# Optimization experiments

Measured on AMD Instinct MI355X. Metric: run time of the kernel, lower is better.

The kernel has to match this reference:

```python
import jax, jax.numpy as jnp
import numpy as np

N, IN_C, OUT_C = 8192, 256, 256


def setup_inputs() -> dict:
    key = jax.random.key(0)
    ks = jax.random.split(key, 12)
    p = lambda k, shape: (jax.random.normal(k, shape, jnp.float32) * 0.05)
    return {
        "X": jax.random.normal(ks[0], (IN_C,), jnp.float32),
        "head": 100,
        "tail": 7,
        "E": jax.random.uniform(ks[1], (N, N), jnp.float32),
        "H": jax.random.normal(ks[2], (N, OUT_C), jnp.float32),
        "W_x_z": p(ks[3], (IN_C, OUT_C)),
        "W_h_z": p(ks[4], (OUT_C, OUT_C)),
        "conv_z": p(ks[5], (OUT_C, OUT_C)),
        "b_z": jnp.zeros((1, OUT_C), jnp.float32),
        "W_x_r": p(ks[6], (IN_C, OUT_C)),
        "W_h_r": p(ks[7], (OUT_C, OUT_C)),
        "conv_r": p(ks[8], (OUT_C, OUT_C)),
        "b_r": jnp.zeros((1, OUT_C), jnp.float32),
        "W_x_h": p(ks[9], (IN_C, OUT_C)),
        "W_h_h": p(ks[10], (OUT_C, OUT_C)),
        "b_h": jnp.zeros((1, OUT_C), jnp.float32),
    }


def reference(X, head, tail, E, H, W_x_z, W_h_z, conv_z, b_z,
              W_x_r, W_h_r, conv_r, b_r, W_x_h, W_h_h, b_h):
    # --- edge-weight update ---
    # Original: M = 0.5*I with M[head,tail]=0.5; Ep = E with Ep[head,tail]+=1;
    # E_new = M @ Ep.  M@Ep scales every row by 0.5 and (if head!=tail) adds
    # 0.5*Ep[tail] into row `head`.  Same math, O(N^2) instead of O(N^3).
    Ep = E.at[head, tail].add(1.0)
    E_new = 0.5 * Ep
    if head != tail:  # head/tail are Python ints (static)
        E_new = E_new.at[head].add(0.5 * Ep[tail])

    h_head = H[head]                 # [OUT_C]
    agg = E_new[head] @ H            # GCN aggregation over neighbors: [OUT_C]

    Z = jax.nn.sigmoid(X @ W_x_z + h_head @ W_h_z + agg @ conv_z + b_z[0])
    R = jax.nn.sigmoid(X @ W_x_r + h_head @ W_h_r + agg @ conv_r + b_r[0])
    H_tilde = jnp.tanh(X @ W_x_h + (h_head * R) @ W_h_h + b_h[0])

    H_new = H.at[head].set(Z * h_head + (1.0 - Z) * H_tilde)
    return E_new, H_new
```

## Files before the change

### kernel.cpp

```cpp
#include <hip/hip_runtime.h>
#include <math.h>

#define NN 8192
#define CC 256
#define LOG2N 13

typedef float f32x4 __attribute__((ext_vector_type(4)));

#define ACC_Z  0
#define ACC_R  256
#define ACC_XH 512
#define ACC_HH 768

#define NAGG    128
#define NMV     20
#define CHAIN   (NAGG + NMV)
#define NSTREAM 2048

__global__ void __launch_bounds__(256) k1(
        const float* __restrict__ X, const float* __restrict__ E,
        const float* __restrict__ H,
        const int* __restrict__ dh, const int* __restrict__ dt,
        const float* __restrict__ Wxz, const float* __restrict__ Whz,
        const float* __restrict__ Cz,  const float* __restrict__ Wxr,
        const float* __restrict__ Whr, const float* __restrict__ Cr,
        const float* __restrict__ Wxh,
        float* __restrict__ acc_ws, float* __restrict__ out) {
    const int bid = blockIdx.x;
    const int t = threadIdx.x;
    const int head = dh[0], tail = dt[0];
    const size_t nn = (size_t)NN * NN;

    if (bid >= CHAIN) {
        const size_t total4 = nn >> 2;
        const size_t step = (size_t)NSTREAM * 256;
        size_t idx = (size_t)(bid - CHAIN) * 256 + t;
        for (; idx < total4; idx += 2 * step) {
            const size_t e0 = idx << 2;
            const size_t e1 = (idx + step) << 2;
            const f32x4 a = __builtin_nontemporal_load((const f32x4*)(E + e0));
            const f32x4 b = __builtin_nontemporal_load((const f32x4*)(E + e1));
            {
                f32x4 o = a * 0.5f;
                const int i = (int)(e0 >> LOG2N);
                if (i == head) {
                    const int j = (int)(e0 & (NN - 1));
                    if (head != tail) {
                        const f32x4 w = *(const f32x4*)(E + (size_t)tail * NN + j);
                        o += w * 0.5f;
                    }
                    if (tail >= j && tail < j + 4) o[tail - j] += 0.5f;
                }
                *(f32x4*)(out + e0) = o;
            }
            {
                f32x4 o = b * 0.5f;
                const int i = (int)(e1 >> LOG2N);
                if (i == head) {
                    const int j = (int)(e1 & (NN - 1));
                    if (head != tail) {
                        const f32x4 w = *(const f32x4*)(E + (size_t)tail * NN + j);
                        o += w * 0.5f;
                    }
                    if (tail >= j && tail < j + 4) o[tail - j] += 0.5f;
                }
                *(f32x4*)(out + e1) = o;
            }
        }
        return;
    }

    if (bid < NAGG) {
        __shared__ float e_sh[64];
        __shared__ f32x4 red[4][64];
        __shared__ float agg_sh[CC];
        const int i0 = bid * 64;
        if (t < 64) {
            const int i = i0 + t;
            float e = 0.5f * E[(size_t)head * NN + i];
            if (head != tail) e += 0.5f * E[(size_t)tail * NN + i];
            if (i == tail) e += 0.5f;
            e_sh[t] = e;
        }
        __syncthreads();
        const int g = t >> 6, c = (t & 63) << 2;
        f32x4 acc = {0.f, 0.f, 0.f, 0.f};
        #pragma unroll
        for (int it = 0; it < 16; ++it) {
            const int r = it * 4 + g;
            const int row = i0 + r;
            const f32x4 hv = *(const f32x4*)(H + (size_t)row * CC + c);
            acc += hv * e_sh[r];
            if (row != head)
                *(f32x4*)(out + nn + (size_t)row * CC + c) = hv;
        }
        red[g][t & 63] = acc;
        __syncthreads();
        if (g == 0) {
            const f32x4 s = red[0][t] + red[1][t] + red[2][t] + red[3][t];
            *(f32x4*)(agg_sh + (t << 2)) = s;
        }
        __syncthreads();
        float pz = 0.f, pr = 0.f;
        #pragma unroll 8
        for (int k = 0; k < CC; ++k) {
            const float a = agg_sh[k];
            pz += a * Cz[(size_t)k * CC + t];
            pr += a * Cr[(size_t)k * CC + t];
        }
        atomicAdd(&acc_ws[ACC_Z + t], pz);
        atomicAdd(&acc_ws[ACC_R + t], pr);
        return;
    }

    {
        const int mb = bid - NAGG;
        const int m = mb >> 2, q = mb & 3;
        __shared__ float v_sh[64];
        const float* W;
        float* dst;
        switch (m) {
            case 0: W = Wxz; dst = acc_ws + ACC_Z; break;
            case 1: W = Whz; dst = acc_ws + ACC_Z; break;
            case 2: W = Wxr; dst = acc_ws + ACC_R; break;
            case 3: W = Whr; dst = acc_ws + ACC_R; break;
            default: W = Wxh; dst = acc_ws + ACC_XH; break;
        }
        if (t < 64) {
            const int k = q * 64 + t;
            v_sh[t] = (m == 1 || m == 3) ? H[(size_t)head * CC + k] : X[k];
        }
        __syncthreads();
        float acc = 0.f;
        #pragma unroll
        for (int kk = 0; kk < 64; ++kk)
            acc += v_sh[kk] * W[(size_t)(q * 64 + kk) * CC + t];
        atomicAdd(&dst[t], acc);
    }
}

__global__ void __launch_bounds__(256) k2(
        const float* __restrict__ H, const int* __restrict__ dh,
        const float* __restrict__ br, const float* __restrict__ Whh,
        float* __restrict__ acc_ws) {
    __shared__ float rs_sh[CC];
    const int t = threadIdx.x;
    const int head = dh[0];
    const float sr = br[t] + acc_ws[ACC_R + t];
    const float r = 1.f / (1.f + expf(-sr));
    rs_sh[t] = H[(size_t)head * CC + t] * r;
    __syncthreads();
    const int k0 = blockIdx.x * 8;
    float acc = 0.f;
    #pragma unroll
    for (int j = 0; j < 8; ++j)
        acc += rs_sh[k0 + j] * Whh[(size_t)(k0 + j) * CC + t];
    atomicAdd(&acc_ws[ACC_HH + t], acc);
}

__global__ void __launch_bounds__(256) k3(
        const float* __restrict__ H, const int* __restrict__ dh,
        const float* __restrict__ bz, const float* __restrict__ bh,
        const float* __restrict__ acc_ws, float* __restrict__ out) {
    const int t = threadIdx.x;
    const int head = dh[0];
    const float z = 1.f / (1.f + expf(-(bz[t] + acc_ws[ACC_Z + t])));
    const float ht = tanhf(bh[t] + acc_ws[ACC_XH + t] + acc_ws[ACC_HH + t]);
    const float h = H[(size_t)head * CC + t];
    out[(size_t)NN * NN + (size_t)head * CC + t] = z * h + (1.f - z) * ht;
}

extern "C" void kernel_launch(void* const* d_in, const int* in_sizes, int n_in,
                              void* d_out, int out_size, void* d_ws, size_t ws_size,
                              hipStream_t stream) {
    const float* X    = (const float*)d_in[0];
    const int*   dh   = (const int*)d_in[1];
    const int*   dt   = (const int*)d_in[2];
    const float* E    = (const float*)d_in[3];
    const float* H    = (const float*)d_in[4];
    const float* Wxz  = (const float*)d_in[5];
    const float* Whz  = (const float*)d_in[6];
    const float* Cz   = (const float*)d_in[7];
    const float* bz   = (const float*)d_in[8];
    const float* Wxr  = (const float*)d_in[9];
    const float* Whr  = (const float*)d_in[10];
    const float* Cr   = (const float*)d_in[11];
    const float* br   = (const float*)d_in[12];
    const float* Wxh  = (const float*)d_in[13];
    const float* Whh  = (const float*)d_in[14];
    const float* bh   = (const float*)d_in[15];
    float* out = (float*)d_out;
    float* acc_ws = (float*)d_ws;

    hipMemsetAsync(acc_ws, 0, 1024 * sizeof(float), stream);
    k1<<<CHAIN + NSTREAM, 256, 0, stream>>>(
        X, E, H, dh, dt, Wxz, Whz, Cz, Wxr, Whr, Cr, Wxh, acc_ws, out);
    k2<<<32, 256, 0, stream>>>(H, dh, br, Whh, acc_ws);
    k3<<<1, 256, 0, stream>>>(H, dh, bz, bh, acc_ws, out);
}
```

Measured before the change: 112.7 us.

## Fuse GRU tail into streaming kernel with dynamic chunk scheduling and last-block finish

Merges the three launches into one kernel. Blocks first do their GRU partial matvec work, then pull fixed-size chunks of the E copy from a global atomic counter, prefetching the next chunk index. A done-counter elects the last block to compute the Whh matvec and final H row, which removes the k2/k3 launches. The grid shrinks to 2048 blocks, so the GRU work now shares blocks with the stream, and there are per-chunk atomics and a serial 256x256 matvec at the tail.

```diff
diff --git a/kernel.cpp b/kernel.cpp
--- a/kernel.cpp
+++ b/kernel.cpp
@@ -10,12 +10,13 @@
 #define ACC_Z  0
 #define ACC_R  256
 #define ACC_XH 512
-#define ACC_HH 768
-
-#define NAGG    128
-#define NMV     20
-#define CHAIN   (NAGG + NMV)
-#define NSTREAM 2048
+
+#define NAGG   128
+#define NMV    20
+#define CHAIN  (NAGG + NMV)
+#define GRID   2048
+#define CHUNK  4096
+#define NCHUNK 4096
 
 __global__ void __launch_bounds__(256) k1(
         const float* __restrict__ X, const float* __restrict__ E,
@@ -24,26 +25,101 @@
         const float* __restrict__ Wxz, const float* __restrict__ Whz,
         const float* __restrict__ Cz,  const float* __restrict__ Wxr,
         const float* __restrict__ Whr, const float* __restrict__ Cr,
-        const float* __restrict__ Wxh,
-        float* __restrict__ acc_ws, float* __restrict__ out) {
+        const float* __restrict__ Wxh, const float* __restrict__ Whh,
+        const float* __restrict__ bz, const float* __restrict__ br,
+        const float* __restrict__ bh,
+        float* __restrict__ ws, float* __restrict__ out) {
     const int bid = blockIdx.x;
     const int t = threadIdx.x;
     const int head = dh[0], tail = dt[0];
     const size_t nn = (size_t)NN * NN;
-
-    if (bid >= CHAIN) {
-        const size_t total4 = nn >> 2;
-        const size_t step = (size_t)NSTREAM * 256;
-        size_t idx = (size_t)(bid - CHAIN) * 256 + t;
-        for (; idx < total4; idx += 2 * step) {
-            const size_t e0 = idx << 2;
-            const size_t e1 = (idx + step) << 2;
+    unsigned* ctr  = (unsigned*)ws + 1024;
+    unsigned* done = (unsigned*)ws + 1056;
+
+    if (bid < NAGG) {
+        __shared__ float e_sh[64];
+        __shared__ f32x4 red[4][64];
+        __shared__ float agg_sh[CC];
+        const int i0 = bid * 64;
+        if (t < 64) {
+            const int i = i0 + t;
+            float e = 0.5f * E[(size_t)head * NN + i];
+            if (head != tail) e += 0.5f * E[(size_t)tail * NN + i];
+            if (i == tail) e += 0.5f;
+            e_sh[t] = e;
+        }
+        __syncthreads();
+        const int g = t >> 6, c = (t & 63) << 2;
+        f32x4 acc = {0.f, 0.f, 0.f, 0.f};
+        #pragma unroll
+        for (int it = 0; it < 16; ++it) {
+            const int r = it * 4 + g;
+            const int row = i0 + r;
+            const f32x4 hv = *(const f32x4*)(H + (size_t)row * CC + c);
+            acc += hv * e_sh[r];
+            if (row != head)
+                *(f32x4*)(out + nn + (size_t)row * CC + c) = hv;
+        }
+        red[g][t & 63] = acc;
+        __syncthreads();
+        if (g == 0) {
+            const f32x4 s = red[0][t] + red[1][t] + red[2][t] + red[3][t];
+            *(f32x4*)(agg_sh + (t << 2)) = s;
+        }
+        __syncthreads();
+        float pz = 0.f, pr = 0.f;
+        #pragma unroll 8
+        for (int k = 0; k < CC; ++k) {
+            const float a = agg_sh[k];
+            pz += a * Cz[(size_t)k * CC + t];
+            pr += a * Cr[(size_t)k * CC + t];
+        }
+        atomicAdd(&ws[ACC_Z + t], pz);
+        atomicAdd(&ws[ACC_R + t], pr);
+        __syncthreads();
+    } else if (bid < CHAIN) {
+        const int mb = bid - NAGG;
+        const int m = mb >> 2, q = mb & 3;
+        __shared__ float v_sh[64];
+        const float* W;
+        int dsto;
+        switch (m) {
+            case 0: W = Wxz; dsto = ACC_Z; break;
+            case 1: W = Whz; dsto = ACC_Z; break;
+            case 2: W = Wxr; dsto = ACC_R; break;
+            case 3: W = Whr; dsto = ACC_R; break;
+            default: W = Wxh; dsto = ACC_XH; break;
+        }
+        if (t < 64) {
+            const int k = q * 64 + t;
+            v_sh[t] = (m == 1 || m == 3) ? H[(size_t)head * CC + k] : X[k];
+        }
+        __syncthreads();
+        float acc = 0.f;
+        #pragma unroll
+        for (int kk = 0; kk < 64; ++kk)
+            acc += v_sh[kk] * W[(size_t)(q * 64 + kk) * CC + t];
+        atomicAdd(&ws[dsto + t], acc);
+        __syncthreads();
+    }
+
+    __shared__ unsigned s_chunk[2];
+    if (t == 0) s_chunk[0] = atomicAdd(ctr, 1u);
+    __syncthreads();
+    unsigned cur = s_chunk[0];
+    int par = 1;
+    while (cur < NCHUNK) {
+        if (t == 0) s_chunk[par] = atomicAdd(ctr, 1u);
+        const size_t base = (size_t)cur * CHUNK + t;
+        #pragma unroll
+        for (int k = 0; k < 16; k += 2) {
+            const size_t e0 = (base + (size_t)k * 256) << 2;
+            const size_t e1 = (base + (size_t)(k + 1) * 256) << 2;
             const f32x4 a = __builtin_nontemporal_load((const f32x4*)(E + e0));
             const f32x4 b = __builtin_nontemporal_load((const f32x4*)(E + e1));
             {
                 f32x4 o = a * 0.5f;
-                const int i = (int)(e0 >> LOG2N);
-                if (i == head) {
+                if ((int)(e0 >> LOG2N) == head) {
                     const int j = (int)(e0 & (NN - 1));
                     if (head != tail) {
                         const f32x4 w = *(const f32x4*)(E + (size_t)tail * NN + j);
@@ -55,8 +131,7 @@
             }
             {
                 f32x4 o = b * 0.5f;
-                const int i = (int)(e1 >> LOG2N);
-                if (i == head) {
+                if ((int)(e1 >> LOG2N) == head) {
                     const int j = (int)(e1 & (NN - 1));
                     if (head != tail) {
                         const f32x4 w = *(const f32x4*)(E + (size_t)tail * NN + j);
@@ -67,107 +142,35 @@
                 *(f32x4*)(out + e1) = o;
             }
         }
-        return;
-    }
-
-    if (bid < NAGG) {
-        __shared__ float e_sh[64];
-        __shared__ f32x4 red[4][64];
-        __shared__ float agg_sh[CC];
-        const int i0 = bid * 64;
-        if (t < 64) {
-            const int i = i0 + t;
-            float e = 0.5f * E[(size_t)head * NN + i];
-            if (head != tail) e += 0.5f * E[(size_t)tail * NN + i];
-            if (i == tail) e += 0.5f;
-            e_sh[t] = e;
-        }
-        __syncthreads();
-        const int g = t >> 6, c = (t & 63) << 2;
-        f32x4 acc = {0.f, 0.f, 0.f, 0.f};
-        #pragma unroll
-        for (int it = 0; it < 16; ++it) {
-            const int r = it * 4 + g;
-            const int row = i0 + r;
-            const f32x4 hv = *(const f32x4*)(H + (size_t)row * CC + c);
-            acc += hv * e_sh[r];
-            if (row != head)
-                *(f32x4*)(out + nn + (size_t)row * CC + c) = hv;
-        }
-        red[g][t & 63] = acc;
-        __syncthreads();
-        if (g == 0) {
-            const f32x4 s = red[0][t] + red[1][t] + red[2][t] + red[3][t];
-            *(f32x4*)(agg_sh + (t << 2)) = s;
-        }
-        __syncthreads();
-        float pz = 0.f, pr = 0.f;
+        __syncthreads();
+        cur = s_chunk[par];
+        par ^= 1;
+    }
+
+    __shared__ int s_last;
+    if (t == 0) {
+        const unsigned old = __hip_atomic_fetch_add(done, 1u, __ATOMIC_ACQ_REL,
+                                                    __HIP_MEMORY_SCOPE_AGENT);
+        s_last = (old == GRID - 1) ? 1 : 0;
+    }
+    __syncthreads();
+    if (s_last) {
+        __shared__ float rs_sh[CC];
+        const float accR = ws[ACC_R + t];
+        const float accZ = ws[ACC_Z + t];
+        const float accXH = ws[ACC_XH + t];
+        const float h = H[(size_t)head * CC + t];
+        const float r = 1.f / (1.f + expf(-(br[t] + accR)));
+        rs_sh[t] = h * r;
+        __syncthreads();
+        float hh = 0.f;
         #pragma unroll 8
-        for (int k = 0; k < CC; ++k) {
-            const float a = agg_sh[k];
-            pz += a * Cz[(size_t)k * CC + t];
-            pr += a * Cr[(size_t)k * CC + t];
-        }
-        atomicAdd(&acc_ws[ACC_Z + t], pz);
-        atomicAdd(&acc_ws[ACC_R + t], pr);
-        return;
-    }
-
-    {
-        const int mb = bid - NAGG;
-        const int m = mb >> 2, q = mb & 3;
-        __shared__ float v_sh[64];
-        const float* W;
-        float* dst;
-        switch (m) {
-            case 0: W = Wxz; dst = acc_ws + ACC_Z; break;
-            case 1: W = Whz; dst = acc_ws + ACC_Z; break;
-            case 2: W = Wxr; dst = acc_ws + ACC_R; break;
-            case 3: W = Whr; dst = acc_ws + ACC_R; break;
-            default: W = Wxh; dst = acc_ws + ACC_XH; break;
-        }
-        if (t < 64) {
-            const int k = q * 64 + t;
-            v_sh[t] = (m == 1 || m == 3) ? H[(size_t)head * CC + k] : X[k];
-        }
-        __syncthreads();
-        float acc = 0.f;
-        #pragma unroll
-        for (int kk = 0; kk < 64; ++kk)
-            acc += v_sh[kk] * W[(size_t)(q * 64 + kk) * CC + t];
-        atomicAdd(&dst[t], acc);
-    }
-}
-
-__global__ void __launch_bounds__(256) k2(
-        const float* __restrict__ H, const int* __restrict__ dh,
-        const float* __restrict__ br, const float* __restrict__ Whh,
-        float* __restrict__ acc_ws) {
-    __shared__ float rs_sh[CC];
-    const int t = threadIdx.x;
-    const int head = dh[0];
-    const float sr = br[t] + acc_ws[ACC_R + t];
-    const float r = 1.f / (1.f + expf(-sr));
-    rs_sh[t] = H[(size_t)head * CC + t] * r;
-    __syncthreads();
-    const int k0 = blockIdx.x * 8;
-    float acc = 0.f;
-    #pragma unroll
-    for (int j = 0; j < 8; ++j)
-        acc += rs_sh[k0 + j] * Whh[(size_t)(k0 + j) * CC + t];
-    atomicAdd(&acc_ws[ACC_HH + t], acc);
-}
-
-__global__ void __launch_bounds__(256) k3(
-        const float* __restrict__ H, const int* __restrict__ dh,
-        const float* __restrict__ bz, const float* __restrict__ bh,
-        const float* __restrict__ acc_ws, float* __restrict__ out) {
-    const int t = threadIdx.x;
-    const int head = dh[0];
-    const float z = 1.f / (1.f + expf(-(bz[t] + acc_ws[ACC_Z + t])));
-    const float ht = tanhf(bh[t] + acc_ws[ACC_XH + t] + acc_ws[ACC_HH + t]);
-    const float h = H[(size_t)head * CC + t];
-    out[(size_t)NN * NN + (size_t)head * CC + t] = z * h + (1.f - z) * ht;
+        for (int k = 0; k < CC; ++k)
+            hh += rs_sh[k] * Whh[(size_t)k * CC + t];
+        const float z = 1.f / (1.f + expf(-(bz[t] + accZ)));
+        const float ht = tanhf(bh[t] + accXH + hh);
+        out[nn + (size_t)head * CC + t] = z * h + (1.f - z) * ht;
+    }
 }
 
 extern "C" void kernel_launch(void* const* d_in, const int* in_sizes, int n_in,
@@ -190,11 +193,10 @@
     const float* Whh  = (const float*)d_in[14];
     const float* bh   = (const float*)d_in[15];
     float* out = (float*)d_out;
-    float* acc_ws = (float*)d_ws;
-
-    hipMemsetAsync(acc_ws, 0, 1024 * sizeof(float), stream);
-    k1<<<CHAIN + NSTREAM, 256, 0, stream>>>(
-        X, E, H, dh, dt, Wxz, Whz, Cz, Wxr, Whr, Cr, Wxh, acc_ws, out);
-    k2<<<32, 256, 0, stream>>>(H, dh, br, Whh, acc_ws);
-    k3<<<1, 256, 0, stream>>>(H, dh, bz, bh, acc_ws, out);
+    float* ws  = (float*)d_ws;
+
+    hipMemsetAsync(ws, 0, 8192, stream);
+    k1<<<GRID, 256, 0, stream>>>(
+        X, E, H, dh, dt, Wxz, Whz, Cz, Wxr, Whr, Cr, Wxh, Whh,
+        bz, br, bh, ws, out);
 }
```

Result: slower. 213.8 us (+89.7%).
